# Performance work log

Hardware: AMD Instinct MI355X
Metric: run time of the kernel (lower is better)

The kernel has to match this reference:

```python
import jax, jax.numpy as jnp
import numpy as np

EPS_NORM = 1e-12  # torch F.normalize eps
EPS_BN = 1e-5     # torch BatchNorm default eps


def l2norm(v, axis=-1):
    n = jnp.sqrt(jnp.sum(v * v, axis=axis, keepdims=True))
    return v / jnp.maximum(n, EPS_NORM)


def setup_inputs() -> dict:
    key = jax.random.key(0)
    k1, k2 = jax.random.split(key, 2)
    N, C, D, M, K = 4, 8, 196, 128, 64
    x = jax.random.normal(k1, (N, C, D, M), dtype=jnp.float32)
    # centroids ~ U[0,1) as in torch.rand
    centroids = jax.random.uniform(k2, (K, M), dtype=jnp.float32)
    alpha = 1.0
    # _init_params: conv.weight = 2*alpha*centroids (1x1 conv), conv.bias = -alpha*||centroids||
    conv_w = 2.0 * alpha * centroids            # (K, M)
    conv_b = -alpha * jnp.linalg.norm(centroids, axis=1)  # (K,)
    gamma = jnp.ones((C,), dtype=jnp.float32)   # BatchNorm3d(8) affine init
    beta = jnp.zeros((C,), dtype=jnp.float32)
    return {"x": x, "conv_w": conv_w, "conv_b": conv_b,
            "centroids": centroids, "gamma": gamma, "beta": beta}


def reference(x, conv_w, conv_b, centroids, gamma, beta):
    # x: (N, C, D, M) with M = descriptor dim, C must equal 8 (BatchNorm3d(8))
    xn = l2norm(x, axis=-1)  # descriptor-wise L2 norm (normalize_input=True)
    # 1x1 conv over channel axis M -> K cluster logits: (N, K, C, D)
    logits = jnp.einsum('ncdm,km->nkcd', xn, conv_w) + conv_b[None, :, None, None]
    soft_assign = jax.nn.softmax(logits, axis=1)  # over clusters K
    # residual: (N, K, C, D, M)
    residual = xn[:, None, :, :, :] - centroids[None, :, None, None, :]
    residual = residual * soft_assign[..., None]
    # permute to (N, C, D, K, M), intra-normalize over descriptor dim
    vlad = jnp.transpose(residual, (0, 2, 3, 1, 4))
    vlad = l2norm(vlad, axis=-1)
    # BatchNorm3d(8), training mode: stats over (N, D, K, M) per channel C
    mean = jnp.mean(vlad, axis=(0, 2, 3, 4), keepdims=True)
    var = jnp.mean((vlad - mean) ** 2, axis=(0, 2, 3, 4), keepdims=True)
    vlad = (vlad - mean) / jnp.sqrt(var + EPS_BN)
    vlad = vlad * gamma[None, :, None, None, None] + beta[None, :, None, None, None]
    N, C, D, K, M = vlad.shape
    vlad = vlad.reshape(N, C, D, K * M)
    return l2norm(vlad, axis=-1)
```

## Files before the change

kernel.cpp:

```cpp
#include <hip/hip_runtime.h>

#define NB 4
#define CB 8
#define DB 196
#define MBd 128
#define KBc 64
#define ROWS (NB*CB*DB)
#define RPB 7
#define GRID (ROWS/RPB)
#define CNTF 6422528.0f

typedef float floatx4 __attribute__((ext_vector_type(4)));

__device__ __forceinline__ float dot4(floatx4 a, floatx4 b){
    return fmaf(a.x,b.x, fmaf(a.y,b.y, fmaf(a.z,b.z, a.w*b.w)));
}

__global__ __launch_bounds__(256) void k_stats(const float* __restrict__ x,
                                               const float* __restrict__ cent,
                                               float* __restrict__ rn_ws,
                                               float* __restrict__ xrn_ws,
                                               float* __restrict__ sv_ws,
                                               float* __restrict__ partial)
{
    __shared__ float cs[KBc*MBd];
    __shared__ float sopc[KBc];
    __shared__ float ssc[KBc];
    __shared__ float sp1[256], sp2[256];
    __shared__ float svp[RPB*4];
    __shared__ float sv7[RPB];

    const int t  = threadIdx.x;
    const int rb = blockIdx.x * RPB;
    const floatx4* c4 = (const floatx4*)cent;
    floatx4* cs4 = (floatx4*)cs;
#pragma unroll
    for (int i = 0; i < 8; ++i) cs4[i*256 + t] = c4[i*256 + t];
    __syncthreads();

    {
        const int kk = t >> 2, q = t & 3;
        const floatx4* crow = &cs4[kk*32 + q*8];
        float ps = 0.f, pc = 0.f;
#pragma unroll
        for (int f = 0; f < 8; ++f) { floatx4 v = crow[f]; ps += (v.x+v.y)+(v.z+v.w); pc += dot4(v,v); }
        sp1[t] = ps; sp2[t] = pc;
    }
    __syncthreads();
    if (t < KBc) {
        ssc[t]  = (sp1[4*t]+sp1[4*t+1])+(sp1[4*t+2]+sp1[4*t+3]);
        sopc[t] = 1.0f + ((sp2[4*t]+sp2[4*t+1])+(sp2[4*t+2]+sp2[4*t+3]));
    }
    __syncthreads();

    const int l = t & 63, w = t >> 6, g = (l >> 4), li = l & 15;
    const floatx4* xg = (const floatx4*)x;

    floatx4 nxa = xg[rb*32 + li];
    floatx4 nxb = xg[rb*32 + 16 + li];
    for (int ri = 0; ri < RPB; ++ri) {
        const int row = rb + ri;
        const floatx4 xa = nxa, xb = nxb;
        if (ri + 1 < RPB) {
            nxa = xg[(row+1)*32 + li];
            nxb = xg[(row+1)*32 + 16 + li];
        }
        float s2 = dot4(xa,xa) + dot4(xb,xb);
        float sx = ((xa.x+xa.y)+(xa.z+xa.w)) + ((xb.x+xb.y)+(xb.z+xb.w));
#pragma unroll
        for (int o = 8; o >= 1; o >>= 1) { s2 += __shfl_xor(s2,o,64); sx += __shfl_xor(sx,o,64); }
        const float xrn = __builtin_amdgcn_rsqf(s2);
        const float Sx  = sx * xrn;
        float sva = 0.f;
        floatx4 rn4;
#pragma unroll
        for (int it = 0; it < 4; ++it) {
            const int k = it*16 + w*4 + g;
            float d = dot4(xa, cs4[k*32+li]) + dot4(xb, cs4[k*32+16+li]);
#pragma unroll
            for (int o = 8; o >= 1; o >>= 1) d += __shfl_xor(d,o,64);
            const float dn = xrn * d;
            const float rn = __builtin_amdgcn_rsqf(fmaf(-2.f, dn, sopc[k]));
            rn4[it] = rn;
            sva = fmaf(Sx - ssc[k], rn, sva);
        }
#pragma unroll
        for (int o = 32; o >= 1; o >>= 1) sva += __shfl_xor(sva,o,64);
        if (li == 0) *(floatx4*)&rn_ws[(size_t)row*KBc + (w*4+g)*4] = rn4;
        if (t == 0) xrn_ws[row] = xrn;
        if (l == 0) svp[ri*4 + w] = sva * 0.0625f;
    }
    __syncthreads();
    if (t < RPB) {
        float s = (svp[4*t]+svp[4*t+1])+(svp[4*t+2]+svp[4*t+3]);
        sv_ws[rb + t] = s;
        sv7[t] = s;
    }
    __syncthreads();
    if (t == 0) {
        float s = 0.f;
#pragma unroll
        for (int i = 0; i < RPB; ++i) s += sv7[i];
        partial[blockIdx.x] = s;
    }
}

__global__ __launch_bounds__(256) void k_out(const float* __restrict__ x,
                                             const float* __restrict__ cent,
                                             const float* __restrict__ rn_ws,
                                             const float* __restrict__ xrn_ws,
                                             const float* __restrict__ sv_ws,
                                             const float* __restrict__ partial,
                                             const float* __restrict__ gamma,
                                             const float* __restrict__ beta,
                                             float* __restrict__ out)
{
    __shared__ float sab[2];
    const int t   = threadIdx.x;
    const int row = blockIdx.x;
    const int c   = (row / DB) % CB;
    const int l = t & 63, w = t >> 6, li2 = l & 31, hi = l >> 5;
    const floatx4* c4 = (const floatx4*)cent;
    const floatx4* xg = (const floatx4*)x;

    const floatx4 xa  = xg[row*32 + li2];
    const float   xrn = xrn_ws[row];
    const float   SVr = sv_ws[row];
    floatx4 cv[8];
    float   rnv[8];
#pragma unroll
    for (int it = 0; it < 8; ++it) {
        const int k = it*8 + w*2 + hi;
        cv[it]  = c4[k*32 + li2];
        rnv[it] = rn_ws[(size_t)row*KBc + ((k & 15) << 2) + (k >> 4)];
    }

    if (t < 64) {
        float s1 = 0.f;
        if (t < 56) {
            const int j0 = t, j1 = t + 56;
            const int b0 = (j0/28)*224 + c*28 + (j0%28);
            const int b1 = (j1/28)*224 + c*28 + (j1%28);
            s1 = partial[b0] + partial[b1];
        }
#pragma unroll
        for (int o = 32; o >= 1; o >>= 1) s1 += __shfl_xor(s1,o,64);
        if (t == 0) {
            const float mean = s1 / CNTF;
            const float var  = 0.0078125f - mean*mean;
            const float istd = __builtin_amdgcn_rsqf(var + 1e-5f);
            const float aa = istd * gamma[c];
            const float bb = beta[c] - mean * aa;
            sab[0] = aa; sab[1] = bb;
        }
    }
    __syncthreads();
    const float aa = sab[0], bb = sab[1];

    const float rni = __builtin_amdgcn_rsqf(
        fmaf(2.f*aa*bb, SVr, fmaf(64.f*aa, aa, 8192.f*bb*bb)));
    const float f1  = aa * rni;
    const float c2v = bb * rni;
    const floatx4 va = xa * xrn;

    floatx4* outr = (floatx4*)out + (size_t)row*2048;
#pragma unroll
    for (int it = 0; it < 8; ++it) {
        const int k = it*8 + w*2 + hi;
        const float cc = f1 * rnv[it];
        floatx4 o1;
        o1.x = fmaf(va.x - cv[it].x, cc, c2v);
        o1.y = fmaf(va.y - cv[it].y, cc, c2v);
        o1.z = fmaf(va.z - cv[it].z, cc, c2v);
        o1.w = fmaf(va.w - cv[it].w, cc, c2v);
        outr[k*32 + li2] = o1;
    }
}

__global__ __launch_bounds__(256) void k_stats_f(const float* __restrict__ x,
                                                 const float* __restrict__ cent,
                                                 float* __restrict__ sv_ws,
                                                 float* __restrict__ partial,
                                                 float* __restrict__ opc_ws)
{
    __shared__ float cs[KBc*MBd];
    __shared__ float sopc[KBc];
    __shared__ float ssc[KBc];
    __shared__ float sp1[256], sp2[256];
    __shared__ float svp[RPB*4];
    __shared__ float sv7[RPB];

    const int t  = threadIdx.x;
    const int rb = blockIdx.x * RPB;
    const floatx4* c4 = (const floatx4*)cent;
    floatx4* cs4 = (floatx4*)cs;
#pragma unroll
    for (int i = 0; i < 8; ++i) cs4[i*256 + t] = c4[i*256 + t];
    __syncthreads();
    {
        const int kk = t >> 2, q = t & 3;
        const floatx4* crow = &cs4[kk*32 + q*8];
        float ps = 0.f, pc = 0.f;
#pragma unroll
        for (int f = 0; f < 8; ++f) { floatx4 v = crow[f]; ps += (v.x+v.y)+(v.z+v.w); pc += dot4(v,v); }
        sp1[t] = ps; sp2[t] = pc;
    }
    __syncthreads();
    if (t < KBc) {
        ssc[t]  = (sp1[4*t]+sp1[4*t+1])+(sp1[4*t+2]+sp1[4*t+3]);
        sopc[t] = 1.0f + ((sp2[4*t]+sp2[4*t+1])+(sp2[4*t+2]+sp2[4*t+3]));
    }
    __syncthreads();
    if (blockIdx.x == 0 && t < KBc) opc_ws[t] = sopc[t];

    const int l = t & 63, w = t >> 6, g = (l >> 4), li = l & 15;
    const floatx4* xg = (const floatx4*)x;
    for (int ri = 0; ri < RPB; ++ri) {
        const int row = rb + ri;
        floatx4 xa = xg[row*32 + li];
        floatx4 xb = xg[row*32 + 16 + li];
        float s2 = dot4(xa,xa) + dot4(xb,xb);
        float sx = ((xa.x+xa.y)+(xa.z+xa.w)) + ((xb.x+xb.y)+(xb.z+xb.w));
#pragma unroll
        for (int o = 8; o >= 1; o >>= 1) { s2 += __shfl_xor(s2,o,64); sx += __shfl_xor(sx,o,64); }
        const float xrn = __builtin_amdgcn_rsqf(s2);
        const float Sx  = sx * xrn;
        float sva = 0.f;
#pragma unroll
        for (int it = 0; it < 4; ++it) {
            const int k = it*16 + w*4 + g;
            float d = dot4(xa, cs4[k*32+li]) + dot4(xb, cs4[k*32+16+li]);
#pragma unroll
            for (int o = 8; o >= 1; o >>= 1) d += __shfl_xor(d,o,64);
            const float dn = xrn * d;
            const float rn = __builtin_amdgcn_rsqf(fmaf(-2.f, dn, sopc[k]));
            sva = fmaf(Sx - ssc[k], rn, sva);
        }
#pragma unroll
        for (int o = 32; o >= 1; o >>= 1) sva += __shfl_xor(sva,o,64);
        if (l == 0) svp[ri*4 + w] = sva * 0.0625f;
    }
    __syncthreads();
    if (t < RPB) {
        float s = (svp[4*t]+svp[4*t+1])+(svp[4*t+2]+svp[4*t+3]);
        sv_ws[rb + t] = s;
        sv7[t] = s;
    }
    __syncthreads();
    if (t == 0) {
        float s = 0.f;
#pragma unroll
        for (int i = 0; i < RPB; ++i) s += sv7[i];
        partial[blockIdx.x] = s;
    }
}

__global__ __launch_bounds__(256) void k_out_f(const float* __restrict__ x,
                                               const float* __restrict__ cent,
                                               const float* __restrict__ sv_ws,
                                               const float* __restrict__ partial,
                                               const float* __restrict__ opc_ws,
                                               const float* __restrict__ gamma,
                                               const float* __restrict__ beta,
                                               float* __restrict__ out)
{
    __shared__ float cs[KBc*MBd];
    __shared__ float sopc[KBc];
    __shared__ float sab[2];
    const int t  = threadIdx.x;
    const int rb = blockIdx.x * RPB;
    const int c  = (blockIdx.x / 28) % CB;
    const floatx4* c4 = (const floatx4*)cent;
    floatx4* cs4 = (floatx4*)cs;
#pragma unroll
    for (int i = 0; i < 8; ++i) cs4[i*256 + t] = c4[i*256 + t];
    if (t >= 64 && t < 128) sopc[t-64] = opc_ws[t-64];
    if (t < 64) {
        float s1 = 0.f;
        if (t < 56) {
            const int j0 = t, j1 = t + 56;
            const int b0 = (j0/28)*224 + c*28 + (j0%28);
            const int b1 = (j1/28)*224 + c*28 + (j1%28);
            s1 = partial[b0] + partial[b1];
        }
#pragma unroll
        for (int o = 32; o >= 1; o >>= 1) s1 += __shfl_xor(s1,o,64);
        if (t == 0) {
            const float mean = s1 / CNTF;
            const float var  = 0.0078125f - mean*mean;
            const float istd = __builtin_amdgcn_rsqf(var + 1e-5f);
            const float aa = istd * gamma[c];
            const float bb = beta[c] - mean * aa;
            sab[0] = aa; sab[1] = bb;
        }
    }
    __syncthreads();
    const float aa = sab[0], bb = sab[1];

    const int l = t & 63, w = t >> 6, g = (l >> 4), li = l & 15;
    const floatx4* xg = (const floatx4*)x;
    for (int ri = 0; ri < RPB; ++ri) {
        const int row = rb + ri;
        floatx4 xa = xg[row*32 + li];
        floatx4 xb = xg[row*32 + 16 + li];
        float s2 = dot4(xa,xa) + dot4(xb,xb);
#pragma unroll
        for (int o = 8; o >= 1; o >>= 1) s2 += __shfl_xor(s2,o,64);
        const float xrn = __builtin_amdgcn_rsqf(s2);
        const floatx4 va = xa * xrn, vb = xb * xrn;
        const float SVr = sv_ws[row];
        const float q   = fmaf(64.f*aa, aa, fmaf(2.f*aa*bb, SVr, 8192.f*bb*bb));
        const float rni = __builtin_amdgcn_rsqf(q);
        const float f1  = aa * rni;
        const float c2  = bb * rni;
        floatx4* outr = (floatx4*)out + (size_t)row*2048;
#pragma unroll
        for (int it = 0; it < 4; ++it) {
            const int k = it*16 + w*4 + g;
            const floatx4 cca = cs4[k*32+li];
            const floatx4 ccb = cs4[k*32+16+li];
            float d = dot4(va,cca) + dot4(vb,ccb);
#pragma unroll
            for (int o = 8; o >= 1; o >>= 1) d += __shfl_xor(d,o,64);
            const float rn = __builtin_amdgcn_rsqf(fmaf(-2.f, d, sopc[k]));
            const float cc = f1 * rn;
            floatx4 o1, o2;
            o1.x = fmaf(va.x - cca.x, cc, c2); o1.y = fmaf(va.y - cca.y, cc, c2);
            o1.z = fmaf(va.z - cca.z, cc, c2); o1.w = fmaf(va.w - cca.w, cc, c2);
            o2.x = fmaf(vb.x - ccb.x, cc, c2); o2.y = fmaf(vb.y - ccb.y, cc, c2);
            o2.z = fmaf(vb.z - ccb.z, cc, c2); o2.w = fmaf(vb.w - ccb.w, cc, c2);
            outr[k*32 + li]      = o1;
            outr[k*32 + 16 + li] = o2;
        }
    }
}

extern "C" void kernel_launch(void* const* d_in, const int* in_sizes, int n_in,
                              void* d_out, int out_size, void* d_ws, size_t ws_size,
                              hipStream_t stream)
{
    const float* x     = (const float*)d_in[0];
    const float* cent  = (const float*)d_in[3];
    const float* gamma = (const float*)d_in[4];
    const float* beta  = (const float*)d_in[5];
    float* out = (float*)d_out;

    const size_t need = (size_t)(ROWS*KBc + ROWS + ROWS + GRID) * sizeof(float);
    if (ws_size >= need) {
        float* rn_ws   = (float*)d_ws;
        float* xrn_ws  = rn_ws + (size_t)ROWS*KBc;
        float* sv_ws   = xrn_ws + ROWS;
        float* partial = sv_ws + ROWS;
        hipLaunchKernelGGL(k_stats, dim3(GRID), dim3(256), 0, stream,
                           x, cent, rn_ws, xrn_ws, sv_ws, partial);
        hipLaunchKernelGGL(k_out,   dim3(ROWS), dim3(256), 0, stream,
                           x, cent, rn_ws, xrn_ws, sv_ws, partial, gamma, beta, out);
    } else {
        float* sv_ws   = (float*)d_ws;
        float* partial = sv_ws + ROWS;
        float* opc_ws  = partial + GRID;
        hipLaunchKernelGGL(k_stats_f, dim3(GRID), dim3(256), 0, stream,
                           x, cent, sv_ws, partial, opc_ws);
        hipLaunchKernelGGL(k_out_f,   dim3(GRID), dim3(256), 0, stream,
                           x, cent, sv_ws, partial, opc_ws, gamma, beta, out);
    }
}
```

Baseline: 53.15 us.

## Restructure stats kernel with transposed LDS centroids and separate BN-coefficient kernel

The stats kernel now stages the centroids transposed in LDS, padded to avoid bank conflicts, with one lane per cluster. Each thread computes full dot products serially over M, which removes the per-cluster shuffle reductions, and each block handles 8 rows instead of 7. The per-channel batch-norm reduction moves out of every output block into a tiny 8-block k_ab kernel that writes scale and shift, so k_out no longer reduces partials and syncs on each row. This adds a third kernel launch and a tiny serial reduction kernel on the critical path.

```diff
diff --git a/kernel.cpp b/kernel.cpp
--- a/kernel.cpp
+++ b/kernel.cpp
@@ -6,6 +6,8 @@
 #define MBd 128
 #define KBc 64
 #define ROWS (NB*CB*DB)
+#define RPB2 8
+#define GRID2 (ROWS/RPB2)
 #define RPB 7
 #define GRID (ROWS/RPB)
 #define CNTF 6422528.0f
@@ -20,88 +22,89 @@
                                                const float* __restrict__ cent,
                                                float* __restrict__ rn_ws,
                                                float* __restrict__ xrn_ws,
-                                               float* __restrict__ sv_ws,
-                                               float* __restrict__ partial)
-{
-    __shared__ float cs[KBc*MBd];
-    __shared__ float sopc[KBc];
-    __shared__ float ssc[KBc];
-    __shared__ float sp1[256], sp2[256];
-    __shared__ float svp[RPB*4];
-    __shared__ float sv7[RPB];
+                                               float* __restrict__ sv_ws)
+{
+    __shared__ floatx4 ct4[32*65];
+    __shared__ floatx4 xs4[RPB2*32];
+    __shared__ float   svbuf[RPB2*65];
 
     const int t  = threadIdx.x;
-    const int rb = blockIdx.x * RPB;
+    const int rb = blockIdx.x * RPB2;
     const floatx4* c4 = (const floatx4*)cent;
-    floatx4* cs4 = (floatx4*)cs;
-#pragma unroll
-    for (int i = 0; i < 8; ++i) cs4[i*256 + t] = c4[i*256 + t];
-    __syncthreads();
-
-    {
-        const int kk = t >> 2, q = t & 3;
-        const floatx4* crow = &cs4[kk*32 + q*8];
-        float ps = 0.f, pc = 0.f;
-#pragma unroll
-        for (int f = 0; f < 8; ++f) { floatx4 v = crow[f]; ps += (v.x+v.y)+(v.z+v.w); pc += dot4(v,v); }
-        sp1[t] = ps; sp2[t] = pc;
-    }
-    __syncthreads();
-    if (t < KBc) {
-        ssc[t]  = (sp1[4*t]+sp1[4*t+1])+(sp1[4*t+2]+sp1[4*t+3]);
-        sopc[t] = 1.0f + ((sp2[4*t]+sp2[4*t+1])+(sp2[4*t+2]+sp2[4*t+3]));
-    }
-    __syncthreads();
-
-    const int l = t & 63, w = t >> 6, g = (l >> 4), li = l & 15;
     const floatx4* xg = (const floatx4*)x;
 
-    floatx4 nxa = xg[rb*32 + li];
-    floatx4 nxb = xg[rb*32 + 16 + li];
-    for (int ri = 0; ri < RPB; ++ri) {
-        const int row = rb + ri;
-        const floatx4 xa = nxa, xb = nxb;
-        if (ri + 1 < RPB) {
-            nxa = xg[(row+1)*32 + li];
-            nxb = xg[(row+1)*32 + 16 + li];
-        }
-        float s2 = dot4(xa,xa) + dot4(xb,xb);
-        float sx = ((xa.x+xa.y)+(xa.z+xa.w)) + ((xb.x+xb.y)+(xb.z+xb.w));
-#pragma unroll
-        for (int o = 8; o >= 1; o >>= 1) { s2 += __shfl_xor(s2,o,64); sx += __shfl_xor(sx,o,64); }
+#pragma unroll
+    for (int i = 0; i < 8; ++i) {
+        const int idx = i*256 + t;
+        const int k = idx >> 5, m4 = idx & 31;
+        ct4[m4*65 + k] = c4[idx];
+    }
+    xs4[t] = xg[rb*32 + t];
+    __syncthreads();
+
+    const int lane = t & 63, w = t >> 6;
+
+    float ssck = 0.f, opck = 1.f;
+#pragma unroll
+    for (int m4 = 0; m4 < 32; ++m4) {
+        const floatx4 cv = ct4[m4*65 + lane];
+        ssck += (cv.x+cv.y)+(cv.z+cv.w);
+        opck  = fmaf(cv.x,cv.x, fmaf(cv.y,cv.y, fmaf(cv.z,cv.z, fmaf(cv.w,cv.w, opck))));
+    }
+
+#pragma unroll
+    for (int rr = 0; rr < 2; ++rr) {
+        const int r   = w*2 + rr;
+        const int row = rb + r;
+        float d = 0.f, s2 = 0.f, sx = 0.f;
+#pragma unroll
+        for (int m4 = 0; m4 < 32; ++m4) {
+            const floatx4 xv = xs4[r*32 + m4];
+            const floatx4 cv = ct4[m4*65 + lane];
+            d  = fmaf(xv.x,cv.x, fmaf(xv.y,cv.y, fmaf(xv.z,cv.z, fmaf(xv.w,cv.w, d))));
+            s2 = fmaf(xv.x,xv.x, fmaf(xv.y,xv.y, fmaf(xv.z,xv.z, fmaf(xv.w,xv.w, s2))));
+            sx += (xv.x+xv.y)+(xv.z+xv.w);
+        }
         const float xrn = __builtin_amdgcn_rsqf(s2);
-        const float Sx  = sx * xrn;
-        float sva = 0.f;
-        floatx4 rn4;
-#pragma unroll
-        for (int it = 0; it < 4; ++it) {
-            const int k = it*16 + w*4 + g;
-            float d = dot4(xa, cs4[k*32+li]) + dot4(xb, cs4[k*32+16+li]);
-#pragma unroll
-            for (int o = 8; o >= 1; o >>= 1) d += __shfl_xor(d,o,64);
-            const float dn = xrn * d;
-            const float rn = __builtin_amdgcn_rsqf(fmaf(-2.f, dn, sopc[k]));
-            rn4[it] = rn;
-            sva = fmaf(Sx - ssc[k], rn, sva);
-        }
-#pragma unroll
-        for (int o = 32; o >= 1; o >>= 1) sva += __shfl_xor(sva,o,64);
-        if (li == 0) *(floatx4*)&rn_ws[(size_t)row*KBc + (w*4+g)*4] = rn4;
-        if (t == 0) xrn_ws[row] = xrn;
-        if (l == 0) svp[ri*4 + w] = sva * 0.0625f;
-    }
-    __syncthreads();
-    if (t < RPB) {
-        float s = (svp[4*t]+svp[4*t+1])+(svp[4*t+2]+svp[4*t+3]);
+        const float rn  = __builtin_amdgcn_rsqf(fmaf(-2.f*xrn, d, opck));
+        rn_ws[(size_t)row*KBc + lane] = rn;
+        if (lane == 0) xrn_ws[row] = xrn;
+        svbuf[r*65 + lane] = (sx*xrn - ssck) * rn;
+    }
+    __syncthreads();
+    if (t < RPB2) {
+        float s = 0.f;
+#pragma unroll
+        for (int j = 0; j < KBc; ++j) s += svbuf[t*65 + j];
         sv_ws[rb + t] = s;
-        sv7[t] = s;
-    }
-    __syncthreads();
+    }
+}
+
+__global__ __launch_bounds__(256) void k_ab(const float* __restrict__ sv_ws,
+                                            const float* __restrict__ gamma,
+                                            const float* __restrict__ beta,
+                                            float* __restrict__ ab_ws)
+{
+    __shared__ float red[256];
+    const int c = blockIdx.x, t = threadIdx.x;
+    float s = 0.f;
+    for (int i = t; i < NB*DB; i += 256) {
+        const int n = i / DB, d = i % DB;
+        s += sv_ws[n*(CB*DB) + c*DB + d];
+    }
+    red[t] = s; __syncthreads();
+#pragma unroll
+    for (int sd = 128; sd >= 1; sd >>= 1) {
+        if (t < sd) red[t] += red[t+sd];
+        __syncthreads();
+    }
     if (t == 0) {
-        float s = 0.f;
-#pragma unroll
-        for (int i = 0; i < RPB; ++i) s += sv7[i];
-        partial[blockIdx.x] = s;
+        const float mean = red[0] / CNTF;
+        const float var  = 0.0078125f - mean*mean;
+        const float istd = __builtin_amdgcn_rsqf(var + 1e-5f);
+        const float aa = istd * gamma[c];
+        ab_ws[2*c]   = aa;
+        ab_ws[2*c+1] = beta[c] - mean * aa;
     }
 }
 
@@ -110,12 +113,9 @@
                                              const float* __restrict__ rn_ws,
                                              const float* __restrict__ xrn_ws,
                                              const float* __restrict__ sv_ws,
-                                             const float* __restrict__ partial,
-                                             const float* __restrict__ gamma,
-                                             const float* __restrict__ beta,
+                                             const float* __restrict__ ab_ws,
                                              float* __restrict__ out)
 {
-    __shared__ float sab[2];
     const int t   = threadIdx.x;
     const int row = blockIdx.x;
     const int c   = (row / DB) % CB;
@@ -126,36 +126,16 @@
     const floatx4 xa  = xg[row*32 + li2];
     const float   xrn = xrn_ws[row];
     const float   SVr = sv_ws[row];
+    const float   aa  = ab_ws[2*c];
+    const float   bb  = ab_ws[2*c+1];
     floatx4 cv[8];
     float   rnv[8];
 #pragma unroll
     for (int it = 0; it < 8; ++it) {
         const int k = it*8 + w*2 + hi;
         cv[it]  = c4[k*32 + li2];
-        rnv[it] = rn_ws[(size_t)row*KBc + ((k & 15) << 2) + (k >> 4)];
-    }
-
-    if (t < 64) {
-        float s1 = 0.f;
-        if (t < 56) {
-            const int j0 = t, j1 = t + 56;
-            const int b0 = (j0/28)*224 + c*28 + (j0%28);
-            const int b1 = (j1/28)*224 + c*28 + (j1%28);
-            s1 = partial[b0] + partial[b1];
-        }
-#pragma unroll
-        for (int o = 32; o >= 1; o >>= 1) s1 += __shfl_xor(s1,o,64);
-        if (t == 0) {
-            const float mean = s1 / CNTF;
-            const float var  = 0.0078125f - mean*mean;
-            const float istd = __builtin_amdgcn_rsqf(var + 1e-5f);
-            const float aa = istd * gamma[c];
-            const float bb = beta[c] - mean * aa;
-            sab[0] = aa; sab[1] = bb;
-        }
-    }
-    __syncthreads();
-    const float aa = sab[0], bb = sab[1];
+        rnv[it] = rn_ws[(size_t)row*KBc + k];
+    }
 
     const float rni = __builtin_amdgcn_rsqf(
         fmaf(2.f*aa*bb, SVr, fmaf(64.f*aa, aa, 8192.f*bb*bb)));
@@ -345,16 +325,18 @@
     const float* beta  = (const float*)d_in[5];
     float* out = (float*)d_out;
 
-    const size_t need = (size_t)(ROWS*KBc + ROWS + ROWS + GRID) * sizeof(float);
+    const size_t need = (size_t)(ROWS*KBc + 2*ROWS + 16) * sizeof(float);
     if (ws_size >= need) {
         float* rn_ws   = (float*)d_ws;
         float* xrn_ws  = rn_ws + (size_t)ROWS*KBc;
         float* sv_ws   = xrn_ws + ROWS;
-        float* partial = sv_ws + ROWS;
-        hipLaunchKernelGGL(k_stats, dim3(GRID), dim3(256), 0, stream,
-                           x, cent, rn_ws, xrn_ws, sv_ws, partial);
-        hipLaunchKernelGGL(k_out,   dim3(ROWS), dim3(256), 0, stream,
-                           x, cent, rn_ws, xrn_ws, sv_ws, partial, gamma, beta, out);
+        float* ab_ws   = sv_ws + ROWS;
+        hipLaunchKernelGGL(k_stats, dim3(GRID2), dim3(256), 0, stream,
+                           x, cent, rn_ws, xrn_ws, sv_ws);
+        hipLaunchKernelGGL(k_ab,    dim3(CB),    dim3(256), 0, stream,
+                           sv_ws, gamma, beta, ab_ws);
+        hipLaunchKernelGGL(k_out,   dim3(ROWS),  dim3(256), 0, stream,
+                           x, cent, rn_ws, xrn_ws, sv_ws, ab_ws, out);
     } else {
         float* sv_ws   = (float*)d_ws;
         float* partial = sv_ws + ROWS;
```

Measured after the change: 59.76 us. +12.4%, slower.
